# Performance work log

Measured on AMD Instinct MI355X. Metric: run time of the kernel, lower is better.

## Reference

```python
import jax, jax.numpy as jnp
import numpy as np

NUM_EMBEDDINGS = 1024
EMBEDDING_DIM = 64
COMMITMENT_COST = 0.25


def setup_inputs() -> dict:
    key = jax.random.key(0)
    k1, k2 = jax.random.split(key)
    z_e = jax.random.normal(k1, (32, 64, 64, 64), dtype=jnp.float32)  # NHWC
    lim = 1.0 / NUM_EMBEDDINGS
    embeddings = jax.random.uniform(
        k2, (NUM_EMBEDDINGS, EMBEDDING_DIM), minval=-lim, maxval=lim, dtype=jnp.float32
    )
    return {"z_e": z_e, "embeddings": embeddings}


def reference(z_e, embeddings):
    D = embeddings.shape[1]
    # Faithful to the TF module: NHWC -> NCHW, then flatten into rows of length D.
    z = jnp.transpose(z_e, (0, 3, 1, 2))            # [B, C, H, W]
    flat = z.reshape(-1, D)                          # [N, D]
    # Squared distances via GEMM (argmin of ||.||^2 == argmin of ||.||); avoids the [N, K, D] tensor.
    d2 = (
        jnp.sum(flat * flat, axis=-1, keepdims=True)
        - 2.0 * flat @ embeddings.T
        + jnp.sum(embeddings * embeddings, axis=-1)
    )                                                # [N, K]
    indices = jnp.argmin(d2, axis=1)                 # [N]
    z_q = embeddings[indices].reshape(z.shape)       # [B, C, H, W]
    z_q_st = z_q + jax.lax.stop_gradient(z - z_q)    # straight-through estimator
    e_latent_loss = jnp.mean((jax.lax.stop_gradient(z_q) - z) ** 2)
    q_latent_loss = jnp.mean((z_q_st - jax.lax.stop_gradient(z)) ** 2)
    loss = q_latent_loss + COMMITMENT_COST * e_latent_loss
    return jnp.transpose(z_q_st, (0, 2, 3, 1)), indices, loss
```

## Files before the change

kernel.cpp:

```cpp
#include <hip/hip_runtime.h>


#define N_Z 8388608
#define N_IDX 131072
#define K_EMB 1024
#define D_EMB 64
#define EPS_GAP 1.25e-4f

typedef __attribute__((ext_vector_type(8))) short bf16x8;
typedef __attribute__((ext_vector_type(4))) float f32x4;

__device__ __forceinline__ unsigned short f2bf(float f) {
  unsigned u = __builtin_bit_cast(unsigned, f);
  unsigned r = 0x7fffu + ((u >> 16) & 1u);
  return (unsigned short)((u + r) >> 16);
}
__device__ __forceinline__ float bf2f(unsigned short b) {
  return __builtin_bit_cast(float, (unsigned)b << 16);
}

__global__ __launch_bounds__(256) void ek2f_kernel(
    const float* __restrict__ emb, float* __restrict__ ek2f) {
  int k = blockIdx.x * 256 + threadIdx.x;
  const float* row = emb + (size_t)k * D_EMB;
  float s = 0.0f;
  for (int d = 0; d < D_EMB; d++) {
    float e = row[d];
    float sq = e * e;
    asm volatile("" : "+v"(sq));
    s = s + sq;
  }
  ek2f[k] = s;
}

__global__ __launch_bounds__(256) void ebf_prep_kernel(
    const float* __restrict__ emb, unsigned short* __restrict__ ehi,
    unsigned short* __restrict__ elo) {
  int gid = blockIdx.x * 256 + threadIdx.x;
  int k = gid >> 3, oct = gid & 7;
  const float* src = emb + (size_t)k * 64 + oct * 8;
  int kt = k >> 4, sp = oct >> 2, l = (oct & 3) * 16 + (k & 15);
  size_t off = ((size_t)((kt * 2 + sp) * 64 + l)) * 8;
  bf16x8 h8, l8;
  #pragma unroll
  for (int i = 0; i < 8; i++) {
    float v = src[i];
    unsigned short hb = f2bf(v);
    float lf = v - bf2f(hb);
    h8[i] = (short)hb;
    l8[i] = (short)f2bf(lf);
  }
  *(bf16x8*)(ehi + off) = h8;
  *(bf16x8*)(elo + off) = l8;
}

#define MFMA_BF16 __builtin_amdgcn_mfma_f32_16x16x32_bf16

__global__ __launch_bounds__(256) void vq_main_kernel(
    const float* __restrict__ z, const float* __restrict__ emb,
    const float* __restrict__ ek2g,
    const unsigned short* __restrict__ ehi_g,
    const unsigned short* __restrict__ elo_g,
    float* __restrict__ out0, float* __restrict__ out_idx,
    double* __restrict__ loss_acc) {
  __shared__ __align__(16) float zts[2][64][64];
  __shared__ float sk2[K_EMB];
  __shared__ float sa[2][64];
  __shared__ int sidx[2][64];
  __shared__ int sflag[2][64];
  __shared__ double lred[16];
  __shared__ float wrv[4];
  __shared__ int wri[4];

  const int t = threadIdx.x;
  const int bid2 = blockIdx.x;
  const int l = t & 63;
  const int cb = (t >> 6) * 16;

  const float4* zt4 = (const float4*)(z + (size_t)bid2 * 8192);
  float4* o4 = (float4*)(out0 + (size_t)bid2 * 8192);
  #pragma unroll
  for (int q = 0; q < 8; q++) {
    int p = t + q * 256;
    float4 v = zt4[p];
    int ti = p >> 10, p4 = p & 1023;
    *(float4*)&zts[ti][p4 >> 4][(p4 & 15) * 4] = v;
    o4[p] = v;
  }
  #pragma unroll
  for (int q = 0; q < 4; q++) sk2[t + q * 256] = ek2g[t + q * 256];
  __syncthreads();

  if (t < 128) {
    int ti = t >> 6, cc = t & 63;
    float a = 0.0f;
    for (int w = 0; w < 64; w++) {
      float zf = zts[ti][w][cc];
      float sq = zf * zf;
      asm volatile("" : "+v"(sq));
      a = a + sq;
    }
    sa[ti][cc] = a;
  }

  bf16x8 zh0_0, zh1_0, zl0_0, zl1_0, zh0_1, zh1_1, zl0_1, zl1_1;
  {
    const int crow = cb + (l & 15);
    const int wb = (l >> 4) * 8;
    #pragma unroll
    for (int i = 0; i < 8; i++) {
      float a0 = zts[0][wb + i][crow];
      unsigned short h0 = f2bf(a0);
      zh0_0[i] = (short)h0; zl0_0[i] = (short)f2bf(a0 - bf2f(h0));
      float a1 = zts[0][32 + wb + i][crow];
      unsigned short h1 = f2bf(a1);
      zh1_0[i] = (short)h1; zl1_0[i] = (short)f2bf(a1 - bf2f(h1));
      float b0 = zts[1][wb + i][crow];
      unsigned short g0 = f2bf(b0);
      zh0_1[i] = (short)g0; zl0_1[i] = (short)f2bf(b0 - bf2f(g0));
      float b1 = zts[1][32 + wb + i][crow];
      unsigned short g1 = f2bf(b1);
      zh1_1[i] = (short)g1; zl1_1[i] = (short)f2bf(b1 - bf2f(g1));
    }
  }
  __syncthreads();

  float A0_[4], A1_[4];
  #pragma unroll
  for (int i = 0; i < 4; i++) {
    A0_[i] = sa[0][cb + (l >> 4) * 4 + i];
    A1_[i] = sa[1][cb + (l >> 4) * 4 + i];
  }

  float m1[2][4], m2[2][4];
  int i1[2][4];
  #pragma unroll
  for (int ti = 0; ti < 2; ti++)
    #pragma unroll
    for (int i = 0; i < 4; i++) { m1[ti][i] = 3.0e38f; m2[ti][i] = 3.0e38f; i1[ti][i] = 0; }

  for (int ch = 0; ch < 16; ch++) {
    #pragma unroll
    for (int t4 = 0; t4 < 4; t4++) {
      const int kt = ch * 4 + t4;
      const size_t fo = (size_t)kt * 1024 + (size_t)l * 8;
      bf16x8 bh0 = *(const bf16x8*)(ehi_g + fo);
      bf16x8 bh1 = *(const bf16x8*)(ehi_g + fo + 512);
      bf16x8 bl0 = *(const bf16x8*)(elo_g + fo);
      bf16x8 bl1 = *(const bf16x8*)(elo_g + fo + 512);

      f32x4 a0 = {0.f, 0.f, 0.f, 0.f}, a1 = {0.f, 0.f, 0.f, 0.f};
      a0 = MFMA_BF16(zh0_0, bh0, a0, 0, 0, 0);
      a1 = MFMA_BF16(zh0_1, bh0, a1, 0, 0, 0);
      a0 = MFMA_BF16(zh1_0, bh1, a0, 0, 0, 0);
      a1 = MFMA_BF16(zh1_1, bh1, a1, 0, 0, 0);
      a0 = MFMA_BF16(zh0_0, bl0, a0, 0, 0, 0);
      a1 = MFMA_BF16(zh0_1, bl0, a1, 0, 0, 0);
      a0 = MFMA_BF16(zh1_0, bl1, a0, 0, 0, 0);
      a1 = MFMA_BF16(zh1_1, bl1, a1, 0, 0, 0);
      a0 = MFMA_BF16(zl0_0, bh0, a0, 0, 0, 0);
      a1 = MFMA_BF16(zl0_1, bh0, a1, 0, 0, 0);
      a0 = MFMA_BF16(zl1_0, bh1, a0, 0, 0, 0);
      a1 = MFMA_BF16(zl1_1, bh1, a1, 0, 0, 0);

      const int k = kt * 16 + (l & 15);
      const float ck = sk2[k];
      #pragma unroll
      for (int i = 0; i < 4; i++) {
        float sc0 = fmaf(-2.0f, a0[i], A0_[i]) + ck;
        if (sc0 < m1[0][i]) { m2[0][i] = m1[0][i]; m1[0][i] = sc0; i1[0][i] = k; }
        else                { m2[0][i] = fminf(m2[0][i], sc0); }
        float sc1 = fmaf(-2.0f, a1[i], A1_[i]) + ck;
        if (sc1 < m1[1][i]) { m2[1][i] = m1[1][i]; m1[1][i] = sc1; i1[1][i] = k; }
        else                { m2[1][i] = fminf(m2[1][i], sc1); }
      }
    }
  }

  #pragma unroll
  for (int ti = 0; ti < 2; ti++) {
    #pragma unroll
    for (int ci = 0; ci < 4; ci++) {
      float v1 = m1[ti][ci], v2 = m2[ti][ci];
      int ix = i1[ti][ci];
      #pragma unroll
      for (int m = 8; m; m >>= 1) {
        float ov1 = __shfl_xor(v1, m, 16);
        int oi1 = __shfl_xor(ix, m, 16);
        float ov2 = __shfl_xor(v2, m, 16);
        if (ov1 < v1)      { v2 = fminf(v1, ov2); v1 = ov1; ix = oi1; }
        else if (ov1 > v1) { v2 = fminf(v2, ov1); }
        else               { v2 = v1; ix = min(ix, oi1); }
      }
      if ((l & 15) == 0) {
        int c = cb + (l >> 4) * 4 + ci;
        sidx[ti][c] = ix;
        sflag[ti][c] = (v2 - v1 <= EPS_GAP) ? 1 : 0;
      }
    }
  }
  __syncthreads();

  #pragma unroll 1
  for (int ti = 0; ti < 2; ti++) {
    #pragma unroll 1
    for (int c = 0; c < 64; c++) {
      if (!sflag[ti][c]) continue;
      float A = sa[ti][c];
      float lm = 3.0e38f;
      int li = 0;
      #pragma unroll
      for (int r = 0; r < 4; r++) {
        int k = t + 256 * r;
        double B = 0.0;
        const float4* e4 = (const float4*)(emb + (size_t)k * 64);
        for (int w4 = 0; w4 < 16; w4++) {
          float4 e = e4[w4];
          B += (double)zts[ti][w4 * 4 + 0][c] * (double)e.x;
          B += (double)zts[ti][w4 * 4 + 1][c] * (double)e.y;
          B += (double)zts[ti][w4 * 4 + 2][c] * (double)e.z;
          B += (double)zts[ti][w4 * 4 + 3][c] * (double)e.w;
        }
        float Bf = (float)B;
        float t1 = A - 2.0f * Bf;
        float sc = t1 + sk2[k];
        if (sc < lm) { lm = sc; li = k; }
      }
      #pragma unroll
      for (int m = 32; m; m >>= 1) {
        float ov = __shfl_xor(lm, m);
        int oi = __shfl_xor(li, m);
        if (ov < lm || (ov == lm && oi < li)) { lm = ov; li = oi; }
      }
      if ((t & 63) == 0) { wrv[t >> 6] = lm; wri[t >> 6] = li; }
      __syncthreads();
      if (t == 0) {
        float bv = wrv[0]; int bi = wri[0];
        #pragma unroll
        for (int q = 1; q < 4; q++) {
          if (wrv[q] < bv || (wrv[q] == bv && wri[q] < bi)) { bv = wrv[q]; bi = wri[q]; }
        }
        sidx[ti][c] = bi;
      }
      __syncthreads();
    }
  }
  __syncthreads();

  if (t < 128) {
    int ti = t >> 6, cc = t & 63;
    int tile = bid2 * 2 + ti;
    int b = tile >> 6, h = tile & 63;
    out_idx[(size_t)b * 4096 + cc * 64 + h] = (float)sidx[ti][cc];
  }

  double ls = 0.0;
  #pragma unroll
  for (int ti = 0; ti < 2; ti++) {
    #pragma unroll
    for (int ci = 0; ci < 4; ci++) {
      int c = (t >> 4) * 4 + ci;
      const float* er = emb + (size_t)sidx[ti][c] * 64;
      #pragma unroll
      for (int s = 0; s < 4; s++) {
        int w = (t & 15) + 16 * s;
        double d = (double)zts[ti][w][c] - (double)er[w];
        ls += d * d;
      }
    }
  }
  #pragma unroll
  for (int m = 8; m; m >>= 1) ls += __shfl_xor(ls, m, 16);
  if ((t & 15) == 0) lred[t >> 4] = ls;
  __syncthreads();
  if (t == 0) {
    double s = 0.0;
    #pragma unroll
    for (int q = 0; q < 16; q++) s += lred[q];
    atomicAdd(loss_acc, s);
  }
}

__global__ void loss_final_kernel(const double* __restrict__ acc,
                                  float* __restrict__ out_loss) {
  *out_loss = (float)(0.25 * (*acc) / (double)N_Z);
}

extern "C" void kernel_launch(void* const* d_in, const int* in_sizes, int n_in,
                              void* d_out, int out_size, void* d_ws, size_t ws_size,
                              hipStream_t stream) {
  const float* z = (const float*)d_in[0];
  const float* emb = (const float*)d_in[1];
  float* out = (float*)d_out;

  float* ek2f = (float*)d_ws;
  double* lacc = (double*)((char*)d_ws + 4096);
  unsigned short* ehi = (unsigned short*)((char*)d_ws + 8192);
  unsigned short* elo = (unsigned short*)((char*)d_ws + 8192 + 131072);

  (void)hipMemsetAsync(lacc, 0, sizeof(double), stream);
  ek2f_kernel<<<4, 256, 0, stream>>>(emb, ek2f);
  ebf_prep_kernel<<<32, 256, 0, stream>>>(emb, ehi, elo);
  vq_main_kernel<<<1024, 256, 0, stream>>>(z, emb, ek2f, ehi, elo,
                                           out, out + N_Z, lacc);
  loss_final_kernel<<<1, 1, 0, stream>>>(lacc, out + N_Z + N_IDX);
}
```

Baseline: 439.7 us.

## Process four row tiles per block with prefetched codebook fragments and compacted rescoring list

Each block now handles four 64-row tiles instead of two. Every codebook bf16 fragment loaded from global memory therefore feeds twice as many MFMAs, and the grid is halved to 512 blocks. The next codebook tile's fragments are software-prefetched into registers during the current iteration. The ambiguous-gap rows are collected into a compact list with a shared atomic counter, so the fp64 rescoring loop no longer scans all flags. The costs are higher register and LDS use (64KB z tile), lower occupancy, and fewer blocks for 256 CUs.

```diff
diff --git a/kernel.cpp b/kernel.cpp
--- a/kernel.cpp
+++ b/kernel.cpp
@@ -63,24 +63,27 @@
     const unsigned short* __restrict__ elo_g,
     float* __restrict__ out0, float* __restrict__ out_idx,
     double* __restrict__ loss_acc) {
-  __shared__ __align__(16) float zts[2][64][64];
+  __shared__ __align__(16) float zts[4][64][64];
   __shared__ float sk2[K_EMB];
-  __shared__ float sa[2][64];
-  __shared__ int sidx[2][64];
-  __shared__ int sflag[2][64];
+  __shared__ float sa[4][64];
+  __shared__ int sidx[4][64];
+  __shared__ int nflag;
+  __shared__ int flist[256];
   __shared__ double lred[16];
   __shared__ float wrv[4];
   __shared__ int wri[4];
 
   const int t = threadIdx.x;
-  const int bid2 = blockIdx.x;
+  const int bid4 = blockIdx.x;
   const int l = t & 63;
   const int cb = (t >> 6) * 16;
 
-  const float4* zt4 = (const float4*)(z + (size_t)bid2 * 8192);
-  float4* o4 = (float4*)(out0 + (size_t)bid2 * 8192);
-  #pragma unroll
-  for (int q = 0; q < 8; q++) {
+  if (t == 0) nflag = 0;
+
+  const float4* zt4 = (const float4*)(z + (size_t)bid4 * 16384);
+  float4* o4 = (float4*)(out0 + (size_t)bid4 * 16384);
+  #pragma unroll
+  for (int q = 0; q < 16; q++) {
     int p = t + q * 256;
     float4 v = zt4[p];
     int ti = p >> 10, p4 = p & 1023;
@@ -91,7 +94,7 @@
   for (int q = 0; q < 4; q++) sk2[t + q * 256] = ek2g[t + q * 256];
   __syncthreads();
 
-  if (t < 128) {
+  {
     int ti = t >> 6, cc = t & 63;
     float a = 0.0f;
     for (int w = 0; w < 64; w++) {
@@ -103,82 +106,84 @@
     sa[ti][cc] = a;
   }
 
-  bf16x8 zh0_0, zh1_0, zl0_0, zl1_0, zh0_1, zh1_1, zl0_1, zl1_1;
+  bf16x8 zh0[4], zh1[4], zl0[4], zl1[4];
   {
     const int crow = cb + (l & 15);
     const int wb = (l >> 4) * 8;
     #pragma unroll
-    for (int i = 0; i < 8; i++) {
-      float a0 = zts[0][wb + i][crow];
-      unsigned short h0 = f2bf(a0);
-      zh0_0[i] = (short)h0; zl0_0[i] = (short)f2bf(a0 - bf2f(h0));
-      float a1 = zts[0][32 + wb + i][crow];
-      unsigned short h1 = f2bf(a1);
-      zh1_0[i] = (short)h1; zl1_0[i] = (short)f2bf(a1 - bf2f(h1));
-      float b0 = zts[1][wb + i][crow];
-      unsigned short g0 = f2bf(b0);
-      zh0_1[i] = (short)g0; zl0_1[i] = (short)f2bf(b0 - bf2f(g0));
-      float b1 = zts[1][32 + wb + i][crow];
-      unsigned short g1 = f2bf(b1);
-      zh1_1[i] = (short)g1; zl1_1[i] = (short)f2bf(b1 - bf2f(g1));
+    for (int ti = 0; ti < 4; ti++) {
+      #pragma unroll
+      for (int i = 0; i < 8; i++) {
+        float v0 = zts[ti][wb + i][crow];
+        unsigned short h0 = f2bf(v0);
+        zh0[ti][i] = (short)h0; zl0[ti][i] = (short)f2bf(v0 - bf2f(h0));
+        float v1 = zts[ti][32 + wb + i][crow];
+        unsigned short h1 = f2bf(v1);
+        zh1[ti][i] = (short)h1; zl1[ti][i] = (short)f2bf(v1 - bf2f(h1));
+      }
     }
   }
   __syncthreads();
 
-  float A0_[4], A1_[4];
-  #pragma unroll
-  for (int i = 0; i < 4; i++) {
-    A0_[i] = sa[0][cb + (l >> 4) * 4 + i];
-    A1_[i] = sa[1][cb + (l >> 4) * 4 + i];
-  }
-
-  float m1[2][4], m2[2][4];
-  int i1[2][4];
-  #pragma unroll
-  for (int ti = 0; ti < 2; ti++)
+  float A_[4][4];
+  #pragma unroll
+  for (int ti = 0; ti < 4; ti++)
+    #pragma unroll
+    for (int i = 0; i < 4; i++) A_[ti][i] = sa[ti][cb + (l >> 4) * 4 + i];
+
+  float m1[4][4], m2[4][4];
+  int i1[4][4];
+  #pragma unroll
+  for (int ti = 0; ti < 4; ti++)
     #pragma unroll
     for (int i = 0; i < 4; i++) { m1[ti][i] = 3.0e38f; m2[ti][i] = 3.0e38f; i1[ti][i] = 0; }
 
-  for (int ch = 0; ch < 16; ch++) {
-    #pragma unroll
-    for (int t4 = 0; t4 < 4; t4++) {
-      const int kt = ch * 4 + t4;
-      const size_t fo = (size_t)kt * 1024 + (size_t)l * 8;
-      bf16x8 bh0 = *(const bf16x8*)(ehi_g + fo);
-      bf16x8 bh1 = *(const bf16x8*)(ehi_g + fo + 512);
-      bf16x8 bl0 = *(const bf16x8*)(elo_g + fo);
-      bf16x8 bl1 = *(const bf16x8*)(elo_g + fo + 512);
-
-      f32x4 a0 = {0.f, 0.f, 0.f, 0.f}, a1 = {0.f, 0.f, 0.f, 0.f};
-      a0 = MFMA_BF16(zh0_0, bh0, a0, 0, 0, 0);
-      a1 = MFMA_BF16(zh0_1, bh0, a1, 0, 0, 0);
-      a0 = MFMA_BF16(zh1_0, bh1, a0, 0, 0, 0);
-      a1 = MFMA_BF16(zh1_1, bh1, a1, 0, 0, 0);
-      a0 = MFMA_BF16(zh0_0, bl0, a0, 0, 0, 0);
-      a1 = MFMA_BF16(zh0_1, bl0, a1, 0, 0, 0);
-      a0 = MFMA_BF16(zh1_0, bl1, a0, 0, 0, 0);
-      a1 = MFMA_BF16(zh1_1, bl1, a1, 0, 0, 0);
-      a0 = MFMA_BF16(zl0_0, bh0, a0, 0, 0, 0);
-      a1 = MFMA_BF16(zl0_1, bh0, a1, 0, 0, 0);
-      a0 = MFMA_BF16(zl1_0, bh1, a0, 0, 0, 0);
-      a1 = MFMA_BF16(zl1_1, bh1, a1, 0, 0, 0);
-
-      const int k = kt * 16 + (l & 15);
-      const float ck = sk2[k];
+  const uint4* hp = (const uint4*)ehi_g;
+  const uint4* lp = (const uint4*)elo_g;
+  uint4 c0 = hp[l], c1 = hp[l + 64], c2 = lp[l], c3 = lp[l + 64];
+  for (int kt = 0; kt < 64; kt++) {
+    uint4 n0 = c0, n1 = c1, n2 = c2, n3 = c3;
+    if (kt < 63) {
+      int nfi = (kt + 1) * 128 + l;
+      n0 = hp[nfi]; n1 = hp[nfi + 64]; n2 = lp[nfi]; n3 = lp[nfi + 64];
+    }
+    bf16x8 bh0 = __builtin_bit_cast(bf16x8, c0);
+    bf16x8 bh1 = __builtin_bit_cast(bf16x8, c1);
+    bf16x8 bl0 = __builtin_bit_cast(bf16x8, c2);
+    bf16x8 bl1 = __builtin_bit_cast(bf16x8, c3);
+
+    f32x4 acc[4];
+    #pragma unroll
+    for (int ti = 0; ti < 4; ti++) acc[ti] = (f32x4){0.f, 0.f, 0.f, 0.f};
+    #pragma unroll
+    for (int ti = 0; ti < 4; ti++) acc[ti] = MFMA_BF16(zh0[ti], bh0, acc[ti], 0, 0, 0);
+    #pragma unroll
+    for (int ti = 0; ti < 4; ti++) acc[ti] = MFMA_BF16(zh1[ti], bh1, acc[ti], 0, 0, 0);
+    #pragma unroll
+    for (int ti = 0; ti < 4; ti++) acc[ti] = MFMA_BF16(zh0[ti], bl0, acc[ti], 0, 0, 0);
+    #pragma unroll
+    for (int ti = 0; ti < 4; ti++) acc[ti] = MFMA_BF16(zh1[ti], bl1, acc[ti], 0, 0, 0);
+    #pragma unroll
+    for (int ti = 0; ti < 4; ti++) acc[ti] = MFMA_BF16(zl0[ti], bh0, acc[ti], 0, 0, 0);
+    #pragma unroll
+    for (int ti = 0; ti < 4; ti++) acc[ti] = MFMA_BF16(zl1[ti], bh1, acc[ti], 0, 0, 0);
+
+    const int k = kt * 16 + (l & 15);
+    const float ck = sk2[k];
+    #pragma unroll
+    for (int ti = 0; ti < 4; ti++) {
       #pragma unroll
       for (int i = 0; i < 4; i++) {
-        float sc0 = fmaf(-2.0f, a0[i], A0_[i]) + ck;
-        if (sc0 < m1[0][i]) { m2[0][i] = m1[0][i]; m1[0][i] = sc0; i1[0][i] = k; }
-        else                { m2[0][i] = fminf(m2[0][i], sc0); }
-        float sc1 = fmaf(-2.0f, a1[i], A1_[i]) + ck;
-        if (sc1 < m1[1][i]) { m2[1][i] = m1[1][i]; m1[1][i] = sc1; i1[1][i] = k; }
-        else                { m2[1][i] = fminf(m2[1][i], sc1); }
-      }
-    }
-  }
-
-  #pragma unroll
-  for (int ti = 0; ti < 2; ti++) {
+        float sc = fmaf(-2.0f, acc[ti][i], A_[ti][i]) + ck;
+        if (sc < m1[ti][i]) { m2[ti][i] = m1[ti][i]; m1[ti][i] = sc; i1[ti][i] = k; }
+        else                { m2[ti][i] = fminf(m2[ti][i], sc); }
+      }
+    }
+    c0 = n0; c1 = n1; c2 = n2; c3 = n3;
+  }
+
+  #pragma unroll
+  for (int ti = 0; ti < 4; ti++) {
     #pragma unroll
     for (int ci = 0; ci < 4; ci++) {
       float v1 = m1[ti][ci], v2 = m2[ti][ci];
@@ -195,68 +200,68 @@
       if ((l & 15) == 0) {
         int c = cb + (l >> 4) * 4 + ci;
         sidx[ti][c] = ix;
-        sflag[ti][c] = (v2 - v1 <= EPS_GAP) ? 1 : 0;
+        if (v2 - v1 <= EPS_GAP) {
+          int pos = atomicAdd(&nflag, 1);
+          flist[pos] = ti * 64 + c;
+        }
       }
     }
   }
   __syncthreads();
 
-  #pragma unroll 1
-  for (int ti = 0; ti < 2; ti++) {
-    #pragma unroll 1
-    for (int c = 0; c < 64; c++) {
-      if (!sflag[ti][c]) continue;
-      float A = sa[ti][c];
-      float lm = 3.0e38f;
-      int li = 0;
-      #pragma unroll
-      for (int r = 0; r < 4; r++) {
-        int k = t + 256 * r;
-        double B = 0.0;
-        const float4* e4 = (const float4*)(emb + (size_t)k * 64);
-        for (int w4 = 0; w4 < 16; w4++) {
-          float4 e = e4[w4];
-          B += (double)zts[ti][w4 * 4 + 0][c] * (double)e.x;
-          B += (double)zts[ti][w4 * 4 + 1][c] * (double)e.y;
-          B += (double)zts[ti][w4 * 4 + 2][c] * (double)e.z;
-          B += (double)zts[ti][w4 * 4 + 3][c] * (double)e.w;
-        }
-        float Bf = (float)B;
-        float t1 = A - 2.0f * Bf;
-        float sc = t1 + sk2[k];
-        if (sc < lm) { lm = sc; li = k; }
-      }
-      #pragma unroll
-      for (int m = 32; m; m >>= 1) {
-        float ov = __shfl_xor(lm, m);
-        int oi = __shfl_xor(li, m);
-        if (ov < lm || (ov == lm && oi < li)) { lm = ov; li = oi; }
-      }
-      if ((t & 63) == 0) { wrv[t >> 6] = lm; wri[t >> 6] = li; }
-      __syncthreads();
-      if (t == 0) {
-        float bv = wrv[0]; int bi = wri[0];
-        #pragma unroll
-        for (int q = 1; q < 4; q++) {
-          if (wrv[q] < bv || (wrv[q] == bv && wri[q] < bi)) { bv = wrv[q]; bi = wri[q]; }
-        }
-        sidx[ti][c] = bi;
-      }
-      __syncthreads();
-    }
-  }
-  __syncthreads();
-
-  if (t < 128) {
+  const int nf = nflag;
+  for (int f = 0; f < nf; f++) {
+    int tc = flist[f];
+    int ti = tc >> 6, c = tc & 63;
+    float A = sa[ti][c];
+    float lm = 3.0e38f;
+    int li = 0;
+    #pragma unroll
+    for (int r = 0; r < 4; r++) {
+      int k = t + 256 * r;
+      double B = 0.0;
+      const float4* e4 = (const float4*)(emb + (size_t)k * 64);
+      for (int w4 = 0; w4 < 16; w4++) {
+        float4 e = e4[w4];
+        B += (double)zts[ti][w4 * 4 + 0][c] * (double)e.x;
+        B += (double)zts[ti][w4 * 4 + 1][c] * (double)e.y;
+        B += (double)zts[ti][w4 * 4 + 2][c] * (double)e.z;
+        B += (double)zts[ti][w4 * 4 + 3][c] * (double)e.w;
+      }
+      float Bf = (float)B;
+      float t1 = A - 2.0f * Bf;
+      float sc = t1 + sk2[k];
+      if (sc < lm) { lm = sc; li = k; }
+    }
+    #pragma unroll
+    for (int m = 32; m; m >>= 1) {
+      float ov = __shfl_xor(lm, m);
+      int oi = __shfl_xor(li, m);
+      if (ov < lm || (ov == lm && oi < li)) { lm = ov; li = oi; }
+    }
+    if ((t & 63) == 0) { wrv[t >> 6] = lm; wri[t >> 6] = li; }
+    __syncthreads();
+    if (t == 0) {
+      float bv = wrv[0]; int bi = wri[0];
+      #pragma unroll
+      for (int q = 1; q < 4; q++) {
+        if (wrv[q] < bv || (wrv[q] == bv && wri[q] < bi)) { bv = wrv[q]; bi = wri[q]; }
+      }
+      sidx[ti][c] = bi;
+    }
+    __syncthreads();
+  }
+
+  {
     int ti = t >> 6, cc = t & 63;
-    int tile = bid2 * 2 + ti;
+    int tile = bid4 * 4 + ti;
     int b = tile >> 6, h = tile & 63;
     out_idx[(size_t)b * 4096 + cc * 64 + h] = (float)sidx[ti][cc];
   }
 
   double ls = 0.0;
   #pragma unroll
-  for (int ti = 0; ti < 2; ti++) {
+  for (int ti = 0; ti < 4; ti++) {
     #pragma unroll
     for (int ci = 0; ci < 4; ci++) {
       int c = (t >> 4) * 4 + ci;
@@ -301,7 +306,7 @@
   (void)hipMemsetAsync(lacc, 0, sizeof(double), stream);
   ek2f_kernel<<<4, 256, 0, stream>>>(emb, ek2f);
   ebf_prep_kernel<<<32, 256, 0, stream>>>(emb, ehi, elo);
-  vq_main_kernel<<<1024, 256, 0, stream>>>(z, emb, ek2f, ehi, elo,
-                                           out, out + N_Z, lacc);
+  vq_main_kernel<<<512, 256, 0, stream>>>(z, emb, ek2f, ehi, elo,
+                                          out, out + N_Z, lacc);
   loss_final_kernel<<<1, 1, 0, stream>>>(lacc, out + N_Z + N_IDX);
 }
```

Result: slower. 650.1 us (+47.8%).
